# Optimization experiments

Hardware: AMD Instinct MI355X
Metric: run time of the kernel (lower is better)

The kernel has to match this reference:

```python
import jax, jax.numpy as jnp
import numpy as np

DIM = 768
HEADS = 12
HEAD_DIM = DIM // HEADS
HIDDEN = 4 * DIM
B, N = 32, 577
EPS = 1e-5


def _layernorm(x, g, b):
    mu = jnp.mean(x, axis=-1, keepdims=True)
    var = jnp.mean(jnp.square(x - mu), axis=-1, keepdims=True)
    return (x - mu) * jax.lax.rsqrt(var + EPS) * g + b


def setup_inputs() -> dict:
    key = jax.random.key(0)
    ks = jax.random.split(key, 8)
    s = lambda fan_in: 1.0 / np.sqrt(fan_in)
    return {
        "x": jax.random.normal(ks[0], (B, N, DIM), jnp.float32),
        "cp_mask": jax.random.uniform(ks[1], (1, 1, N, N), jnp.float32),
        "ln1_g": jnp.ones((DIM,), jnp.float32),
        "ln1_b": jnp.zeros((DIM,), jnp.float32),
        "w_qkv": jax.random.uniform(ks[2], (DIM, 3 * DIM), jnp.float32, -s(DIM), s(DIM)),
        "w_proj": jax.random.uniform(ks[3], (DIM, DIM), jnp.float32, -s(DIM), s(DIM)),
        "b_proj": jnp.zeros((DIM,), jnp.float32),
        "ln2_g": jnp.ones((DIM,), jnp.float32),
        "ln2_b": jnp.zeros((DIM,), jnp.float32),
        "w_fc1": jax.random.uniform(ks[4], (DIM, HIDDEN), jnp.float32, -s(DIM), s(DIM)),
        "b_fc1": jnp.zeros((HIDDEN,), jnp.float32),
        "w_fc2": jax.random.uniform(ks[5], (HIDDEN, DIM), jnp.float32, -s(HIDDEN), s(HIDDEN)),
        "b_fc2": jnp.zeros((DIM,), jnp.float32),
    }


def reference(x, cp_mask, ln1_g, ln1_b, w_qkv, w_proj, b_proj,
              ln2_g, ln2_b, w_fc1, b_fc1, w_fc2, b_fc2):
    scale = HEAD_DIM ** -0.5
    # --- attention branch ---
    h = _layernorm(x, ln1_g, ln1_b)
    qkv = (h @ w_qkv).reshape(B, N, 3, HEADS, HEAD_DIM)
    q, k, v = jnp.moveaxis(qkv, 2, 0)            # each [B,N,H,Dh]
    q = q.transpose(0, 2, 1, 3)                   # [B,H,N,Dh]
    k = k.transpose(0, 2, 1, 3)
    v = v.transpose(0, 2, 1, 3)
    attn = jnp.einsum('bhnd,bhmd->bhnm', q, k) * scale * cp_mask
    attn = jax.nn.softmax(attn, axis=-1)
    out = jnp.einsum('bhnm,bhmd->bhnd', attn, v)
    out = out.transpose(0, 2, 1, 3).reshape(B, N, DIM)
    out = out @ w_proj + b_proj
    x = x + out
    # --- MLP branch ---
    h = _layernorm(x, ln2_g, ln2_b)
    h = jax.nn.gelu(h @ w_fc1 + b_fc1, approximate=False)
    h = h @ w_fc2 + b_fc2
    return x + h
```

## Files before the change

kernel.cpp:

```cpp
#include <hip/hip_runtime.h>
#include <math.h>

typedef unsigned short u16;
typedef unsigned int u32;
typedef __attribute__((ext_vector_type(8))) short bf16x8;
typedef __attribute__((ext_vector_type(4))) float f32x4;

#define B_    32
#define N_    577
#define DIM_  768
#define HEADS_ 12
#define HD_   64
#define HID_  3072
#define MTOT_ (B_*N_)
#define NP_   640

__device__ __forceinline__ u16 f2b(float f){
  u32 u = __builtin_bit_cast(u32, f);
  u += 0x7fffu + ((u >> 16) & 1u);
  return (u16)(u >> 16);
}
__device__ __forceinline__ float b2f(u16 h){
  return __builtin_bit_cast(float, (u32)h << 16);
}

__device__ __forceinline__ void gl_lds16(const void* g, void* l){
  __builtin_amdgcn_global_load_lds(
      (const __attribute__((address_space(1))) u32*)g,
      (__attribute__((address_space(3))) u32*)l, 16, 0, 0);
}
__device__ __forceinline__ void gl_lds4(const void* g, void* l){
  __builtin_amdgcn_global_load_lds(
      (const __attribute__((address_space(1))) u32*)g,
      (__attribute__((address_space(3))) u32*)l, 4, 0, 0);
}

__global__ __launch_bounds__(256) void convT(const float* __restrict__ w,
                                             u16* __restrict__ wt, int K, int N){
  __shared__ float t[32][33];
  int n0 = blockIdx.x * 32, k0 = blockIdx.y * 32;
  int tx = threadIdx.x, ty = threadIdx.y;
  #pragma unroll
  for (int j = 0; j < 4; ++j)
    t[ty + j*8][tx] = w[(size_t)(k0 + ty + j*8) * N + n0 + tx];
  __syncthreads();
  #pragma unroll
  for (int j = 0; j < 4; ++j)
    wt[(size_t)(n0 + ty + j*8) * K + k0 + tx] = f2b(t[tx][ty + j*8]);
}

__global__ __launch_bounds__(256) void ln_k(const float* __restrict__ x,
                                            const float* __restrict__ g,
                                            const float* __restrict__ b,
                                            u16* __restrict__ out){
  int row = blockIdx.x, tid = threadIdx.x;
  const float* xr = x + (size_t)row * DIM_;
  float v0 = xr[tid], v1 = xr[tid + 256], v2 = xr[tid + 512];
  float s = v0 + v1 + v2;
  float s2 = v0*v0 + v1*v1 + v2*v2;
  #pragma unroll
  for (int m = 1; m < 64; m <<= 1){ s += __shfl_xor(s, m); s2 += __shfl_xor(s2, m); }
  __shared__ float ws[8];
  int wid = tid >> 6, ln = tid & 63;
  if (ln == 0){ ws[wid] = s; ws[4 + wid] = s2; }
  __syncthreads();
  s  = ws[0] + ws[1] + ws[2] + ws[3];
  s2 = ws[4] + ws[5] + ws[6] + ws[7];
  float mu = s * (1.0f / DIM_);
  float var = s2 * (1.0f / DIM_) - mu * mu;
  float rs = rsqrtf(var + 1e-5f);
  u16* orow = out + (size_t)row * DIM_;
  orow[tid]       = f2b((v0 - mu) * rs * g[tid]       + b[tid]);
  orow[tid + 256] = f2b((v1 - mu) * rs * g[tid + 256] + b[tid + 256]);
  orow[tid + 512] = f2b((v2 - mu) * rs * g[tid + 512] + b[tid + 512]);
}

#define BM 128
#define BN 128
#define BK 32

template<int EPI>
__global__ __launch_bounds__(256) void gemm_bt(
    const u16* __restrict__ A, const u16* __restrict__ Bt,
    int M, int N, int K,
    const float* __restrict__ bias,
    const float* __restrict__ resid,
    float* __restrict__ outf,
    u16* __restrict__ outb,
    u16* __restrict__ qb, u16* __restrict__ kb, u16* __restrict__ vtb)
{
  __shared__ u16 Al[BM * BK];
  __shared__ u16 Bl[BN * BK];
  int tid = threadIdx.x;
  int wid = tid >> 6, l = tid & 63, ln = l & 15, sub = l >> 4;
  int wm = wid >> 1, wn = wid & 1;
  int tm = blockIdx.x, tn = blockIdx.y;

  f32x4 acc[4][4] = {};
  int arow = tid >> 2;
  int acol = (tid & 3) * 8;

  int gr0 = tm * BM + arow;      if (gr0 >= M) gr0 = M - 1;
  int gr1 = tm * BM + arow + 64; if (gr1 >= M) gr1 = M - 1;
  const u16* ga0 = A + (size_t)gr0 * K + acol;
  const u16* ga1 = A + (size_t)gr1 * K + acol;
  const u16* gb0 = Bt + (size_t)(tn * BN + arow) * K + acol;
  const u16* gb1 = Bt + (size_t)(tn * BN + arow + 64) * K + acol;
  u16* la0 = &Al[arow * BK + acol];
  u16* la1 = &Al[(arow + 64) * BK + acol];
  u16* lb0 = &Bl[arow * BK + acol];
  u16* lb1 = &Bl[(arow + 64) * BK + acol];

  const int ktiles = K / BK;
  for (int kt = 0; kt < ktiles; ++kt){
    int kbase = kt * BK;
    gl_lds16(ga0 + kbase, la0);
    gl_lds16(ga1 + kbase, la1);
    gl_lds16(gb0 + kbase, lb0);
    gl_lds16(gb1 + kbase, lb1);
    __syncthreads();
    bf16x8 af[4], bfr[4];
    #pragma unroll
    for (int mi = 0; mi < 4; ++mi) af[mi]  = *(const bf16x8*)&Al[(wm*64 + mi*16 + ln) * BK + sub*8];
    #pragma unroll
    for (int ni = 0; ni < 4; ++ni) bfr[ni] = *(const bf16x8*)&Bl[(wn*64 + ni*16 + ln) * BK + sub*8];
    #pragma unroll
    for (int mi = 0; mi < 4; ++mi)
      #pragma unroll
      for (int ni = 0; ni < 4; ++ni)
        acc[mi][ni] = __builtin_amdgcn_mfma_f32_16x16x32_bf16(af[mi], bfr[ni], acc[mi][ni], 0, 0, 0);
    __syncthreads();
  }

  #pragma unroll
  for (int mi = 0; mi < 4; ++mi){
    int rbase = tm * BM + wm * 64 + mi * 16 + sub * 4;
    #pragma unroll
    for (int ni = 0; ni < 4; ++ni){
      int col = tn * BN + wn * 64 + ni * 16 + ln;
      #pragma unroll
      for (int r = 0; r < 4; ++r){
        int grow = rbase + r;
        if (grow >= M) continue;
        float val = acc[mi][ni][r];
        if (EPI == 0){
          u32 bb = (u32)grow / 577u;
          u32 nn = (u32)grow - bb * 577u;
          int which = col / 768;
          int rem = col - which * 768;
          int hh = rem >> 6;
          int d  = col & 63;
          if (which == 0)
            qb[(((size_t)bb * HEADS_ + hh) * N_ + nn) * HD_ + d] = f2b(val);
          else if (which == 1)
            kb[(((size_t)bb * HEADS_ + hh) * N_ + nn) * HD_ + d] = f2b(val);
          else
            vtb[(((size_t)bb * HEADS_ + hh) * HD_ + d) * NP_ + nn] = f2b(val);
        } else if (EPI == 1){
          outf[(size_t)grow * N + col] = val + bias[col] + resid[(size_t)grow * N + col];
        } else {
          float t = val + bias[col];
          float ge = 0.5f * t * (1.0f + erff(t * 0.70710678118654752f));
          outb[(size_t)grow * N + col] = f2b(ge);
        }
      }
    }
  }
}

__global__ __launch_bounds__(256) void attn_k(
    const u16* __restrict__ q, const u16* __restrict__ k,
    const u16* __restrict__ vt, const float* __restrict__ mask,
    u16* __restrict__ o)
{
  const float SCALE = 0.125f;
  int qt = blockIdx.x, bh = blockIdx.y;
  int tid = threadIdx.x;
  int wid = tid >> 6, l = tid & 63, ln = l & 15, sub = l >> 4;
  int b = bh / HEADS_, hh = bh - b * HEADS_;
  int qrow0_blk = qt * 64;
  int qrow0 = qrow0_blk + wid * 16;

  __shared__ u16 Kl[64 * 64];
  __shared__ u16 Vl[64 * 64];
  __shared__ float Ml[64 * 64];
  __shared__ u16 Pl[4][16 * 64];

  int qr = qrow0 + ln; if (qr > N_ - 1) qr = N_ - 1;
  const u16* qbase = q + ((size_t)bh * N_ + qr) * HD_;
  bf16x8 qf0 = *(const bf16x8*)&qbase[sub * 8];
  bf16x8 qf1 = *(const bf16x8*)&qbase[32 + sub * 8];

  f32x4 oacc[4] = {};
  float mrun[4] = {-1e30f, -1e30f, -1e30f, -1e30f};
  float lrun[4] = {0.f, 0.f, 0.f, 0.f};

  for (int mt = 0; mt < 10; ++mt){
    int mbase = mt * 64;
    #pragma unroll
    for (int p = 0; p < 2; ++p){
      int row = (tid >> 3) + p * 32;
      int sc = (tid & 7) ^ (row & 7);
      int kr = mbase + row; if (kr > N_ - 1) kr = N_ - 1;
      gl_lds16(&k[((size_t)bh * N_ + kr) * HD_ + sc * 8], &Kl[row * 64 + (tid & 7) * 8]);
      gl_lds16(&vt[((size_t)bh * HD_ + row) * NP_ + mbase + sc * 8], &Vl[row * 64 + (tid & 7) * 8]);
    }
    if (mbase + 63 < N_){
      #pragma unroll
      for (int p = 0; p < 4; ++p){
        int row = (tid >> 4) + p * 16;
        int grow = qrow0_blk + row; if (grow > N_ - 1) grow = N_ - 1;
        gl_lds16(&mask[(size_t)grow * N_ + mbase + (tid & 15) * 4], &Ml[row * 64 + (tid & 15) * 4]);
      }
    } else {
      #pragma unroll
      for (int p = 0; p < 16; ++p){
        int row = (tid >> 6) + p * 4;
        int grow = qrow0_blk + row; if (grow > N_ - 1) grow = N_ - 1;
        int gcol = mbase + (tid & 63); if (gcol > N_ - 1) gcol = N_ - 1;
        gl_lds4(&mask[(size_t)grow * N_ + gcol], &Ml[row * 64 + (tid & 63)]);
      }
    }
    __syncthreads();

    f32x4 s[4];
    #pragma unroll
    for (int c = 0; c < 4; ++c){
      int krow = c * 16 + ln;
      bf16x8 kf0 = *(const bf16x8*)&Kl[krow * 64 + ((sub    ) ^ (krow & 7)) * 8];
      bf16x8 kf1 = *(const bf16x8*)&Kl[krow * 64 + ((4 + sub) ^ (krow & 7)) * 8];
      f32x4 z = {};
      z = __builtin_amdgcn_mfma_f32_16x16x32_bf16(qf0, kf0, z, 0, 0, 0);
      z = __builtin_amdgcn_mfma_f32_16x16x32_bf16(qf1, kf1, z, 0, 0, 0);
      s[c] = z;
    }
    #pragma unroll
    for (int c = 0; c < 4; ++c){
      int mg = mbase + c * 16 + ln;
      #pragma unroll
      for (int r = 0; r < 4; ++r){
        if (mg < N_)
          s[c][r] = s[c][r] * SCALE * Ml[(sub * 4 + r) * 64 + c * 16 + ln];
        else
          s[c][r] = -1e30f;
      }
    }
    float pm[4];
    #pragma unroll
    for (int r = 0; r < 4; ++r)
      pm[r] = fmaxf(fmaxf(s[0][r], s[1][r]), fmaxf(s[2][r], s[3][r]));
    #pragma unroll
    for (int m = 1; m < 16; m <<= 1){
      #pragma unroll
      for (int r = 0; r < 4; ++r) pm[r] = fmaxf(pm[r], __shfl_xor(pm[r], m));
    }
    float alpha[4];
    #pragma unroll
    for (int r = 0; r < 4; ++r){
      float mnew = fmaxf(mrun[r], pm[r]);
      alpha[r] = __expf(mrun[r] - mnew);
      mrun[r] = mnew;
    }
    float ps[4] = {0.f, 0.f, 0.f, 0.f};
    #pragma unroll
    for (int c = 0; c < 4; ++c)
      #pragma unroll
      for (int r = 0; r < 4; ++r){
        float p = __expf(s[c][r] - mrun[r]);
        s[c][r] = p;
        ps[r] += p;
      }
    #pragma unroll
    for (int m = 1; m < 16; m <<= 1){
      #pragma unroll
      for (int r = 0; r < 4; ++r) ps[r] += __shfl_xor(ps[r], m);
    }
    #pragma unroll
    for (int r = 0; r < 4; ++r) lrun[r] = lrun[r] * alpha[r] + ps[r];
    #pragma unroll
    for (int c = 0; c < 4; ++c)
      #pragma unroll
      for (int r = 0; r < 4; ++r){
        int prow = sub * 4 + r;
        int pcol = c * 16 + ln;
        Pl[wid][prow * 64 + (((pcol >> 3) ^ (prow & 7)) << 3) + (pcol & 7)] = f2b(s[c][r]);
      }
    #pragma unroll
    for (int dt = 0; dt < 4; ++dt)
      #pragma unroll
      for (int r = 0; r < 4; ++r) oacc[dt][r] *= alpha[r];
    #pragma unroll
    for (int half = 0; half < 2; ++half){
      bf16x8 pa = *(const bf16x8*)&Pl[wid][ln * 64 + (((half * 4 + sub) ^ (ln & 7)) << 3)];
      #pragma unroll
      for (int dt = 0; dt < 4; ++dt){
        int vrow = dt * 16 + ln;
        bf16x8 vf = *(const bf16x8*)&Vl[vrow * 64 + (((half * 4 + sub) ^ (vrow & 7)) << 3)];
        oacc[dt] = __builtin_amdgcn_mfma_f32_16x16x32_bf16(pa, vf, oacc[dt], 0, 0, 0);
      }
    }
    __syncthreads();
  }
  float inv[4];
  #pragma unroll
  for (int r = 0; r < 4; ++r) inv[r] = 1.0f / lrun[r];
  #pragma unroll
  for (int dt = 0; dt < 4; ++dt)
    #pragma unroll
    for (int r = 0; r < 4; ++r){
      int qg = qrow0 + sub * 4 + r;
      if (qg < N_)
        o[((size_t)b * N_ + qg) * DIM_ + hh * HD_ + dt * 16 + ln] = f2b(oacc[dt][r] * inv[r]);
    }
}

#define OFF_WQKV  0ull
#define OFF_WPROJ 3538944ull
#define OFF_WFC1  4718592ull
#define OFF_WFC2  9437184ull
#define OFF_BUFA  14155776ull
#define OFF_BUFB  (OFF_BUFA + 28360704ull)
#define OFF_BUFC  (OFF_BUFB + 28360704ull)
#define OFF_VT    (OFF_BUFC + 28360704ull)

extern "C" void kernel_launch(void* const* d_in, const int* in_sizes, int n_in,
                              void* d_out, int out_size, void* d_ws, size_t ws_size,
                              hipStream_t stream)
{
  const float* x     = (const float*)d_in[0];
  const float* mask  = (const float*)d_in[1];
  const float* ln1g  = (const float*)d_in[2];
  const float* ln1b  = (const float*)d_in[3];
  const float* wqkv  = (const float*)d_in[4];
  const float* wproj = (const float*)d_in[5];
  const float* bproj = (const float*)d_in[6];
  const float* ln2g  = (const float*)d_in[7];
  const float* ln2b  = (const float*)d_in[8];
  const float* wfc1  = (const float*)d_in[9];
  const float* bfc1  = (const float*)d_in[10];
  const float* wfc2  = (const float*)d_in[11];
  const float* bfc2  = (const float*)d_in[12];
  float* out = (float*)d_out;

  char* ws = (char*)d_ws;
  u16* wqkv_t  = (u16*)(ws + OFF_WQKV);
  u16* wproj_t = (u16*)(ws + OFF_WPROJ);
  u16* wfc1_t  = (u16*)(ws + OFF_WFC1);
  u16* wfc2_t  = (u16*)(ws + OFF_WFC2);
  u16* hbuf  = (u16*)(ws + OFF_BUFA);
  u16* obuf  = (u16*)(ws + OFF_BUFA);
  u16* qbuf  = (u16*)(ws + OFF_BUFB);
  u16* h2buf = (u16*)(ws + OFF_BUFB);
  u16* kbuf  = (u16*)(ws + OFF_BUFC);
  u16* vtbuf = (u16*)(ws + OFF_VT);
  u16* h3buf = (u16*)(ws + OFF_BUFC);

  dim3 tb(32, 8);
  convT<<<dim3(2304/32, 768/32), tb, 0, stream>>>(wqkv,  wqkv_t,  768,  2304);
  convT<<<dim3(768/32,  768/32), tb, 0, stream>>>(wproj, wproj_t, 768,  768);
  convT<<<dim3(3072/32, 768/32), tb, 0, stream>>>(wfc1,  wfc1_t,  768,  3072);
  convT<<<dim3(768/32, 3072/32), tb, 0, stream>>>(wfc2,  wfc2_t,  3072, 768);

  ln_k<<<MTOT_, 256, 0, stream>>>(x, ln1g, ln1b, hbuf);

  gemm_bt<0><<<dim3(145, 18), 256, 0, stream>>>(hbuf, wqkv_t, MTOT_, 2304, 768,
      nullptr, nullptr, nullptr, nullptr, qbuf, kbuf, vtbuf);

  attn_k<<<dim3(10, 384), 256, 0, stream>>>(qbuf, kbuf, vtbuf, mask, obuf);

  gemm_bt<1><<<dim3(145, 6), 256, 0, stream>>>(obuf, wproj_t, MTOT_, 768, 768,
      bproj, x, out, nullptr, nullptr, nullptr, nullptr);

  ln_k<<<MTOT_, 256, 0, stream>>>(out, ln2g, ln2b, h2buf);

  const int M0 = 9216, M1 = MTOT_ - M0;
  gemm_bt<2><<<dim3(72, 24), 256, 0, stream>>>(h2buf, wfc1_t, M0, 3072, 768,
      bfc1, nullptr, nullptr, h3buf, nullptr, nullptr, nullptr);
  gemm_bt<1><<<dim3(72, 6), 256, 0, stream>>>(h3buf, wfc2_t, M0, 768, 3072,
      bfc2, out, out, nullptr, nullptr, nullptr, nullptr);
  gemm_bt<2><<<dim3(73, 24), 256, 0, stream>>>(h2buf + (size_t)M0 * 768, wfc1_t, M1, 3072, 768,
      bfc1, nullptr, nullptr, h3buf, nullptr, nullptr, nullptr);
  gemm_bt<1><<<dim3(73, 6), 256, 0, stream>>>(h3buf, wfc2_t, M1, 768, 3072,
      bfc2, out + (size_t)M0 * 768, out + (size_t)M0 * 768, nullptr, nullptr, nullptr, nullptr);
}
```

Before: 980.2 us.

## Transpose attention score layout, swizzle mask LDS, remap GEMM tiles per XCD

The attention kernel now computes K·Q^T so each lane owns one query row. Softmax max and sum then need only two cross-lane shuffles instead of sixteen-wide butterflies. The mask tile is XOR-swizzled in LDS and read as float4, and P is packed with v_cvt_pk_bf16_f32 into 32-bit LDS stores. The GEMM remaps workgroup IDs so consecutive tiles land on the same XCD for better L2 reuse, and the attention grid is reordered so heads vary fastest. These changes trade extra shuffles for alpha and normalization broadcast and add more complex indexing.

```diff
diff --git a/kernel.cpp b/kernel.cpp
--- a/kernel.cpp
+++ b/kernel.cpp
@@ -20,8 +20,10 @@
   u += 0x7fffu + ((u >> 16) & 1u);
   return (u16)(u >> 16);
 }
-__device__ __forceinline__ float b2f(u16 h){
-  return __builtin_bit_cast(float, (u32)h << 16);
+__device__ __forceinline__ u32 cvtpk(float lo, float hi){
+  u32 r;
+  asm("v_cvt_pk_bf16_f32 %0, %1, %2" : "=v"(r) : "v"(lo), "v"(hi));
+  return r;
 }
 
 __device__ __forceinline__ void gl_lds16(const void* g, void* l){
@@ -94,7 +96,14 @@
   int tid = threadIdx.x;
   int wid = tid >> 6, l = tid & 63, ln = l & 15, sub = l >> 4;
   int wm = wid >> 1, wn = wid & 1;
-  int tm = blockIdx.x, tn = blockIdx.y;
+
+  int nwg  = gridDim.x * gridDim.y;
+  int flat = blockIdx.x + gridDim.x * blockIdx.y;
+  int q8 = nwg >> 3, r8 = nwg & 7;
+  int xcd = flat & 7, j8 = flat >> 3;
+  int wgid = (xcd < r8 ? xcd * (q8 + 1) : r8 * (q8 + 1) + (xcd - r8) * q8) + j8;
+  int tm = wgid / gridDim.y;
+  int tn = wgid - tm * gridDim.y;
 
   f32x4 acc[4][4] = {};
   int arow = tid >> 2;
@@ -174,7 +183,7 @@
     u16* __restrict__ o)
 {
   const float SCALE = 0.125f;
-  int qt = blockIdx.x, bh = blockIdx.y;
+  int bh = blockIdx.x, qt = blockIdx.y;
   int tid = threadIdx.x;
   int wid = tid >> 6, l = tid & 63, ln = l & 15, sub = l >> 4;
   int b = bh / HEADS_, hh = bh - b * HEADS_;
@@ -192,8 +201,7 @@
   bf16x8 qf1 = *(const bf16x8*)&qbase[32 + sub * 8];
 
   f32x4 oacc[4] = {};
-  float mrun[4] = {-1e30f, -1e30f, -1e30f, -1e30f};
-  float lrun[4] = {0.f, 0.f, 0.f, 0.f};
+  float mrun = -1e30f, lrun = 0.f;
 
   for (int mt = 0; mt < 10; ++mt){
     int mbase = mt * 64;
@@ -210,15 +218,18 @@
       for (int p = 0; p < 4; ++p){
         int row = (tid >> 4) + p * 16;
         int grow = qrow0_blk + row; if (grow > N_ - 1) grow = N_ - 1;
-        gl_lds16(&mask[(size_t)grow * N_ + mbase + (tid & 15) * 4], &Ml[row * 64 + (tid & 15) * 4]);
+        int sc = (tid & 15) ^ (row & 15);
+        gl_lds16(&mask[(size_t)grow * N_ + mbase + sc * 4], &Ml[row * 64 + (tid & 15) * 4]);
       }
     } else {
       #pragma unroll
       for (int p = 0; p < 16; ++p){
         int row = (tid >> 6) + p * 4;
         int grow = qrow0_blk + row; if (grow > N_ - 1) grow = N_ - 1;
-        int gcol = mbase + (tid & 63); if (gcol > N_ - 1) gcol = N_ - 1;
-        gl_lds4(&mask[(size_t)grow * N_ + gcol], &Ml[row * 64 + (tid & 63)]);
+        int kp = tid & 63;
+        int lcol = ((((kp >> 2) ^ (row & 15)) << 2) | (kp & 3));
+        int gcol = mbase + lcol; if (gcol > N_ - 1) gcol = N_ - 1;
+        gl_lds4(&mask[(size_t)grow * N_ + gcol], &Ml[row * 64 + kp]);
       }
     }
     __syncthreads();
@@ -230,87 +241,81 @@
       bf16x8 kf0 = *(const bf16x8*)&Kl[krow * 64 + ((sub    ) ^ (krow & 7)) * 8];
       bf16x8 kf1 = *(const bf16x8*)&Kl[krow * 64 + ((4 + sub) ^ (krow & 7)) * 8];
       f32x4 z = {};
-      z = __builtin_amdgcn_mfma_f32_16x16x32_bf16(qf0, kf0, z, 0, 0, 0);
-      z = __builtin_amdgcn_mfma_f32_16x16x32_bf16(qf1, kf1, z, 0, 0, 0);
+      z = __builtin_amdgcn_mfma_f32_16x16x32_bf16(kf0, qf0, z, 0, 0, 0);
+      z = __builtin_amdgcn_mfma_f32_16x16x32_bf16(kf1, qf1, z, 0, 0, 0);
       s[c] = z;
     }
+    int mrow = wid * 16 + ln;
     #pragma unroll
     for (int c = 0; c < 4; ++c){
-      int mg = mbase + c * 16 + ln;
+      f32x4 mv = *(const f32x4*)&Ml[mrow * 64 + (((c * 4 + sub) ^ ln) << 2)];
+      int mg0 = mbase + c * 16 + sub * 4;
       #pragma unroll
       for (int r = 0; r < 4; ++r){
-        if (mg < N_)
-          s[c][r] = s[c][r] * SCALE * Ml[(sub * 4 + r) * 64 + c * 16 + ln];
-        else
-          s[c][r] = -1e30f;
-      }
-    }
-    float pm[4];
-    #pragma unroll
-    for (int r = 0; r < 4; ++r)
-      pm[r] = fmaxf(fmaxf(s[0][r], s[1][r]), fmaxf(s[2][r], s[3][r]));
-    #pragma unroll
-    for (int m = 1; m < 16; m <<= 1){
-      #pragma unroll
-      for (int r = 0; r < 4; ++r) pm[r] = fmaxf(pm[r], __shfl_xor(pm[r], m));
-    }
-    float alpha[4];
-    #pragma unroll
-    for (int r = 0; r < 4; ++r){
-      float mnew = fmaxf(mrun[r], pm[r]);
-      alpha[r] = __expf(mrun[r] - mnew);
-      mrun[r] = mnew;
-    }
-    float ps[4] = {0.f, 0.f, 0.f, 0.f};
+        if (mg0 + r < N_) s[c][r] = s[c][r] * SCALE * mv[r];
+        else              s[c][r] = -1e30f;
+      }
+    }
+    float pm = s[0][0];
     #pragma unroll
     for (int c = 0; c < 4; ++c)
       #pragma unroll
+      for (int r = 0; r < 4; ++r) pm = fmaxf(pm, s[c][r]);
+    pm = fmaxf(pm, __shfl_xor(pm, 16));
+    pm = fmaxf(pm, __shfl_xor(pm, 32));
+    float mnew = fmaxf(mrun, pm);
+    float alpha = __expf(mrun - mnew);
+    mrun = mnew;
+    float ps = 0.f;
+    #pragma unroll
+    for (int c = 0; c < 4; ++c)
+      #pragma unroll
       for (int r = 0; r < 4; ++r){
-        float p = __expf(s[c][r] - mrun[r]);
+        float p = __expf(s[c][r] - mrun);
         s[c][r] = p;
-        ps[r] += p;
-      }
-    #pragma unroll
-    for (int m = 1; m < 16; m <<= 1){
-      #pragma unroll
-      for (int r = 0; r < 4; ++r) ps[r] += __shfl_xor(ps[r], m);
-    }
-    #pragma unroll
-    for (int r = 0; r < 4; ++r) lrun[r] = lrun[r] * alpha[r] + ps[r];
+        ps += p;
+      }
+    ps += __shfl_xor(ps, 16);
+    ps += __shfl_xor(ps, 32);
+    lrun = lrun * alpha + ps;
     #pragma unroll
     for (int c = 0; c < 4; ++c)
       #pragma unroll
-      for (int r = 0; r < 4; ++r){
-        int prow = sub * 4 + r;
-        int pcol = c * 16 + ln;
-        Pl[wid][prow * 64 + (((pcol >> 3) ^ (prow & 7)) << 3) + (pcol & 7)] = f2b(s[c][r]);
-      }
+      for (int h = 0; h < 2; ++h){
+        int kk = c * 16 + sub * 4 + 2 * h;
+        u32 w = cvtpk(s[c][2 * h], s[c][2 * h + 1]);
+        *(u32*)&Pl[wid][ln * 64 + (((kk >> 3) ^ (ln & 7)) << 3) + (kk & 7)] = w;
+      }
+    float a_d[4];
+    #pragma unroll
+    for (int r = 0; r < 4; ++r) a_d[r] = __shfl(alpha, sub * 4 + r);
     #pragma unroll
     for (int dt = 0; dt < 4; ++dt)
       #pragma unroll
-      for (int r = 0; r < 4; ++r) oacc[dt][r] *= alpha[r];
-    #pragma unroll
-    for (int half = 0; half < 2; ++half){
-      bf16x8 pa = *(const bf16x8*)&Pl[wid][ln * 64 + (((half * 4 + sub) ^ (ln & 7)) << 3)];
+      for (int r = 0; r < 4; ++r) oacc[dt][r] *= a_d[r];
+    #pragma unroll
+    for (int kbv = 0; kbv < 2; ++kbv){
+      bf16x8 pa = *(const bf16x8*)&Pl[wid][ln * 64 + (((kbv * 4 + sub) ^ (ln & 7)) << 3)];
       #pragma unroll
       for (int dt = 0; dt < 4; ++dt){
         int vrow = dt * 16 + ln;
-        bf16x8 vf = *(const bf16x8*)&Vl[vrow * 64 + (((half * 4 + sub) ^ (vrow & 7)) << 3)];
+        bf16x8 vf = *(const bf16x8*)&Vl[vrow * 64 + (((kbv * 4 + sub) ^ (vrow & 7)) << 3)];
         oacc[dt] = __builtin_amdgcn_mfma_f32_16x16x32_bf16(pa, vf, oacc[dt], 0, 0, 0);
       }
     }
     __syncthreads();
   }
-  float inv[4];
-  #pragma unroll
-  for (int r = 0; r < 4; ++r) inv[r] = 1.0f / lrun[r];
+  float rinv = 1.0f / lrun;
+  float inv_d[4];
+  #pragma unroll
+  for (int r = 0; r < 4; ++r) inv_d[r] = __shfl(rinv, sub * 4 + r);
   #pragma unroll
   for (int dt = 0; dt < 4; ++dt)
     #pragma unroll
     for (int r = 0; r < 4; ++r){
       int qg = qrow0 + sub * 4 + r;
       if (qg < N_)
-        o[((size_t)b * N_ + qg) * DIM_ + hh * HD_ + dt * 16 + ln] = f2b(oacc[dt][r] * inv[r]);
+        o[((size_t)b * N_ + qg) * DIM_ + hh * HD_ + dt * 16 + ln] = f2b(oacc[dt][r] * inv_d[r]);
     }
 }
 
@@ -366,7 +371,7 @@
   gemm_bt<0><<<dim3(145, 18), 256, 0, stream>>>(hbuf, wqkv_t, MTOT_, 2304, 768,
       nullptr, nullptr, nullptr, nullptr, qbuf, kbuf, vtbuf);
 
-  attn_k<<<dim3(10, 384), 256, 0, stream>>>(qbuf, kbuf, vtbuf, mask, obuf);
+  attn_k<<<dim3(384, 10), 256, 0, stream>>>(qbuf, kbuf, vtbuf, mask, obuf);
 
   gemm_bt<1><<<dim3(145, 6), 256, 0, stream>>>(obuf, wproj_t, MTOT_, 768, 768,
       bproj, x, out, nullptr, nullptr, nullptr, nullptr);
```

Result: faster. 908.0 us (-7.4%).
